# Optimization experiments

Hardware: AMD Instinct MI355X
Metric: run time of the kernel (lower is better)

## Reference

```python
import jax, jax.numpy as jnp
import numpy as np

W = 1024          # hpm.W (Fourier window size)
D = 2 * W         # real-ified dimension
BATCH = 2048
P = 8             # number of previous windows
OMEGA = 50        # sparsity level kept by hard threshold
N_ITERS = 10
L = 1.0           # hpm.L (Lipschitz constant, non-learnable)
CLAMP = 150.0


def setup_inputs() -> dict:
    key = jax.random.key(0)
    k1, k2, k3 = jax.random.split(key, 3)
    x = jax.random.normal(k1, (BATCH, D), jnp.float32)
    prev_windows = jax.random.normal(k2, (P, BATCH, D), jnp.float32)
    # learnable dictionary (Fourier-initialized in the original; random orthogonal-ish here)
    W_d = jax.random.normal(k3, (D, D), jnp.float32) / np.float32(np.sqrt(D))
    # S = I - (1/L) W_d^T W_d, exactly as in __init__
    S = jnp.eye(D, dtype=jnp.float32) - (1.0 / L) * (W_d.T @ W_d)
    lambda2 = jnp.array(1.0, jnp.float32)
    return {"x": x, "prev_windows": prev_windows, "W_d": W_d, "S": S, "lambda2": lambda2}


def _hard_thr(v):
    # keep the OMEGA largest-|.| entries along the last axis, zero the rest
    a = jnp.abs(v)
    kth = jax.lax.top_k(a, OMEGA)[0][..., -1:]  # (batch, 1) threshold
    return jnp.where(a >= kth, v, jnp.zeros_like(v))


def reference(x, prev_windows, W_d, S, lambda2):
    # B = (1/L) W_d x         (batch, D); z vectors kept as (batch, D), last dim == the
    # original dim=-2 since trailing singleton dim is squeezed away.
    B = (1.0 / L) * jnp.einsum('ij,bj->bi', W_d, x)
    z = _hard_thr(B)
    z = _hard_thr(B + jnp.einsum('ij,bj->bi', S, z))

    # attention over previous windows
    s_t = jnp.einsum('ji,bj->bi', W_d, z)                       # W_d^T z : (batch, D)
    s_prev = jnp.einsum('ij,pbj->pbi', W_d, prev_windows)       # (P, batch, D)
    # diagonal of (P,batch,batch) matmul == per-(p,b) dot product; compute it directly
    att = jnp.einsum('pbd,bd->pb', s_prev, s_t)                 # (P, batch)
    att = jax.nn.softmax(att, axis=1)
    pw = jnp.clip(prev_windows, -CLAMP, CLAMP)
    z = lambda2 * jnp.sum(pw * att[..., None], axis=0)          # (batch, D)

    # LIHT iterations; only zs[-1] is used downstream, so carry only the last z
    def step(zc, _):
        zn = _hard_thr(B + jnp.einsum('ij,bj->bi', S, zc))
        return zn, None
    z_last, _ = jax.lax.scan(step, z, None, length=N_ITERS)

    # complex power spectrum: sign flip on imag part does not change the norm
    cpx = z_last.reshape(BATCH, 2, W)
    p = cpx[:, 0, :] ** 2 + cpx[:, 1, :] ** 2                   # (batch, W)
    mD = p.sum(0)                                               # (W,)
    mD_norm = (mD - mD.min()) / (mD.max() - mD.min() + 1e-8)
    return mD_norm, z_last
```

## Files before the change

### kernel.cpp

```cpp
#include <hip/hip_runtime.h>


#define DD 2048
#define NB 2048
#define PLANE ((size_t)1 << 22)
#define ZONE 49152

using short8v  = __attribute__((ext_vector_type(8))) short;
using ushort8v = __attribute__((ext_vector_type(8))) unsigned short;
using ushort4v = __attribute__((ext_vector_type(4))) unsigned short;
using float4v  = __attribute__((ext_vector_type(4))) float;

__device__ __forceinline__ unsigned short f2bf(float f) {
  unsigned u = __float_as_uint(f);
  u = u + 0x7fffu + ((u >> 16) & 1u);
  return (unsigned short)(u >> 16);
}
__device__ __forceinline__ float bf2f(unsigned short h) {
  return __uint_as_float((unsigned)h << 16);
}
__device__ __forceinline__ void gload16(const void* g, void* l) {
  __builtin_amdgcn_global_load_lds((const __attribute__((address_space(1))) void*)g,
                                   (__attribute__((address_space(3))) void*)l,
                                   16, 0, 0);
}

template<int R>
__global__ __launch_bounds__(256)
void conv3T(const float* __restrict__ in, unsigned short* __restrict__ p0,
            unsigned short* __restrict__ p1, unsigned short* __restrict__ p2) {
  __shared__ unsigned short lds3[3][4][R][8];
  const int rt = blockIdx.x, c = blockIdx.y, t = threadIdx.x;
  const int cf = (t & 7) * 4;
  const int g = cf >> 3, e0 = cf & 7;
#pragma unroll
  for (int pass = 0; pass < R / 32; ++pass) {
    const int r = pass * 32 + (t >> 3);
    float4 v = *(const float4*)(in + (size_t)(rt * R + r) * DD + c * 32 + cf);
    float vv[4] = {v.x, v.y, v.z, v.w};
    ushort4v o0, o1, o2;
#pragma unroll
    for (int j = 0; j < 4; ++j) {
      unsigned short a0 = f2bf(vv[j]); float r1 = vv[j] - bf2f(a0);
      unsigned short a1 = f2bf(r1);    float r2 = r1 - bf2f(a1);
      unsigned short a2 = f2bf(r2);
      o0[j] = a0; o1[j] = a1; o2[j] = a2;
    }
    *(ushort4v*)&lds3[0][g][r][e0] = o0;
    *(ushort4v*)&lds3[1][g][r][e0] = o1;
    *(ushort4v*)&lds3[2][g][r][e0] = o2;
  }
  __syncthreads();
  const ushort8v* src = (const ushort8v*)lds3;
  const size_t tb = ((size_t)rt * 64 + c) * (R * 32);
#pragma unroll
  for (int w = 0; w < (3 * R) / 64; ++w) {
    const int idx = w * 256 + t;
    const int p = idx / (4 * R), off = idx % (4 * R);
    unsigned short* dst = (p == 0 ? p0 : p == 1 ? p1 : p2) + tb + (size_t)off * 8;
    *(ushort8v*)dst = src[idx];
  }
}

__global__ __launch_bounds__(256)
void tconv3(const float* __restrict__ in, unsigned short* __restrict__ p0,
            unsigned short* __restrict__ p1, unsigned short* __restrict__ p2) {
  __shared__ unsigned short lds3[3][4][64][8];
  const int nt = blockIdx.x, c = blockIdx.y, t = threadIdx.x;
  const int nf = (t & 15) * 4;
#pragma unroll
  for (int pass = 0; pass < 2; ++pass) {
    const int kr = pass * 16 + (t >> 4);
    float4 v = *(const float4*)(in + (size_t)(c * 32 + kr) * DD + nt * 64 + nf);
    float vv[4] = {v.x, v.y, v.z, v.w};
    const int g = kr >> 3, e = kr & 7;
#pragma unroll
    for (int j = 0; j < 4; ++j) {
      unsigned short a0 = f2bf(vv[j]); float r1 = vv[j] - bf2f(a0);
      unsigned short a1 = f2bf(r1);    float r2 = r1 - bf2f(a1);
      unsigned short a2 = f2bf(r2);
      lds3[0][g][nf + j][e] = a0;
      lds3[1][g][nf + j][e] = a1;
      lds3[2][g][nf + j][e] = a2;
    }
  }
  __syncthreads();
  const ushort8v* src = (const ushort8v*)lds3;
  const size_t tb = ((size_t)nt * 64 + c) * 2048;
#pragma unroll
  for (int w = 0; w < 3; ++w) {
    const int idx = w * 256 + t;
    const int p = idx >> 8, off = idx & 255;
    unsigned short* dst = (p == 0 ? p0 : p == 1 ? p1 : p2) + tb + (size_t)off * 8;
    *(ushort8v*)dst = src[idx];
  }
}

template<int ADD>
__global__ __launch_bounds__(512)
void gemm_bf6(const unsigned short* __restrict__ PA,
              const unsigned short* __restrict__ PB,
              const float* __restrict__ Cadd, float* __restrict__ Cout) {
  __shared__ char lds[3 * ZONE];
  const int tid = threadIdx.x, lane = tid & 63, wid = tid >> 6;

  const int lin = (int)blockIdx.x;
  const int xcd = lin & 7, q = lin >> 3;
  const int mt = (xcd >> 1) * 4 + (q >> 3);
  const int nt = (xcd & 1) * 8 + (q & 7);
  const int m0 = mt * 128, n0 = nt * 128;

  auto stage = [&](char* base, int c) {
    if (wid < 4) {
      const size_t at = ((size_t)mt * 64 + c) * 4096;
#pragma unroll
      for (int i = 0; i < 6; ++i) {
        const int slot = wid * 6 + i, p = slot >> 3, j = slot & 7;
        gload16(PA + p * PLANE + at + j * 512 + lane * 8,
                base + p * 8192 + j * 1024 + lane * 16);
      }
    } else {
#pragma unroll
      for (int i = 0; i < 6; ++i) {
        const int b = (wid - 4) * 6 + i, p = b >> 3, r = b & 7;
        const int sub = r >> 2, j = r & 3;
        const size_t bt = ((size_t)(nt * 2 + sub) * 64 + c) * 2048;
        gload16(PB + p * PLANE + bt + j * 512 + lane * 8,
                base + 24576 + p * 8192 + sub * 4096 + j * 1024 + lane * 16);
      }
    }
  };

  float4v acc[4][2] = {};

  const int rsel = (wid >> 2) * 64;
  const int csel = (wid & 3) * 32;
  const int g16  = lane >> 4;
  const int l15  = lane & 15;
  const int aoff = g16 * 2048 + (rsel + l15) * 16;
  const int boff = 24576 + (csel >> 6) * 4096 + g16 * 1024
                 + ((csel & 32) + l15) * 16;

  stage(lds, 0);
  stage(lds + ZONE, 1);

  int zc = 0, zs = 2;
  for (int c = 0; c < 64; ++c) {
    if (c + 2 < 64) stage(lds + zs * ZONE, c + 2);
    if (c + 2 < 64)      asm volatile("s_waitcnt vmcnt(12)" ::: "memory");
    else if (c + 1 < 64) asm volatile("s_waitcnt vmcnt(6)"  ::: "memory");
    else                 asm volatile("s_waitcnt vmcnt(0)"  ::: "memory");
    __builtin_amdgcn_s_barrier();
    __builtin_amdgcn_sched_barrier(0);

    const char* cur = lds + zc * ZONE;
    short8v b0[2], b1[2], b2[2];
#pragma unroll
    for (int ng = 0; ng < 2; ++ng) {
      b0[ng] = *(const short8v*)(cur + boff + 0 * 8192 + ng * 256);
      b1[ng] = *(const short8v*)(cur + boff + 1 * 8192 + ng * 256);
      b2[ng] = *(const short8v*)(cur + boff + 2 * 8192 + ng * 256);
    }
#pragma unroll
    for (int mg = 0; mg < 4; ++mg) {
      const short8v a0 = *(const short8v*)(cur + 0 * 8192 + aoff + mg * 256);
      const short8v a1 = *(const short8v*)(cur + 1 * 8192 + aoff + mg * 256);
      const short8v a2 = *(const short8v*)(cur + 2 * 8192 + aoff + mg * 256);
#pragma unroll
      for (int ng = 0; ng < 2; ++ng) {
        float4v t = acc[mg][ng];
        t = __builtin_amdgcn_mfma_f32_16x16x32_bf16(a0, b0[ng], t, 0, 0, 0);
        t = __builtin_amdgcn_mfma_f32_16x16x32_bf16(a0, b1[ng], t, 0, 0, 0);
        t = __builtin_amdgcn_mfma_f32_16x16x32_bf16(a1, b0[ng], t, 0, 0, 0);
        t = __builtin_amdgcn_mfma_f32_16x16x32_bf16(a1, b1[ng], t, 0, 0, 0);
        t = __builtin_amdgcn_mfma_f32_16x16x32_bf16(a0, b2[ng], t, 0, 0, 0);
        t = __builtin_amdgcn_mfma_f32_16x16x32_bf16(a2, b0[ng], t, 0, 0, 0);
        acc[mg][ng] = t;
      }
    }
    __builtin_amdgcn_sched_barrier(0);
    __builtin_amdgcn_s_barrier();
    zc = (zc == 2) ? 0 : zc + 1;
    zs = (zs == 2) ? 0 : zs + 1;
  }

  const int row0 = m0 + rsel + g16 * 4;
  const int col0 = n0 + csel + l15;
#pragma unroll
  for (int mg = 0; mg < 4; ++mg)
#pragma unroll
    for (int ng = 0; ng < 2; ++ng)
#pragma unroll
      for (int r = 0; r < 4; ++r) {
        const size_t o = (size_t)(row0 + mg * 16 + r) * DD + col0 + ng * 16;
        float v = acc[mg][ng][r];
        if (ADD) v += Cadd[o];
        Cout[o] = v;
      }
}

template<int HASBASE>
__global__ __launch_bounds__(64)
void spapply_sl(const float* __restrict__ M, const float* __restrict__ baseB,
                float* __restrict__ outF, const unsigned* __restrict__ sidx,
                const float* __restrict__ sval, const int* __restrict__ scnt) {
  const int b = blockIdx.y, lane = threadIdx.x;
  const int col = blockIdx.x * 256 + lane * 4;
  const int nc = scnt[b];
  const unsigned* ip = sidx + b * 64;
  const float* vp = sval + b * 64;
  const size_t ro = (size_t)b * DD + col;
  float4 a;
  if (HASBASE) a = *(const float4*)&baseB[ro];
  else         a = make_float4(0.f, 0.f, 0.f, 0.f);
  for (int t = 0; t < nc; ++t) {
    const unsigned j = ip[t];
    const float v = vp[t];
    float4 m = *(const float4*)&M[(size_t)j * DD + col];
    a.x = fmaf(v, m.x, a.x); a.y = fmaf(v, m.y, a.y);
    a.z = fmaf(v, m.z, a.z); a.w = fmaf(v, m.w, a.w);
  }
  *(float4*)&outF[ro] = a;
}

__global__ __launch_bounds__(64)
void topk_kernel(const float* __restrict__ src, unsigned* __restrict__ sidx,
                 float* __restrict__ sval, int* __restrict__ scnt,
                 float* __restrict__ dense, float* __restrict__ mD,
                 int finalMode) {
  const int b = blockIdx.x;
  const int lane = threadIdx.x;
  const float* row = src + (size_t)b * DD;
  float v[32]; unsigned ab[32];
#pragma unroll
  for (int e4 = 0; e4 < 8; ++e4) {
    float4 t = *(const float4*)&row[e4*256 + lane*4];
    v[e4*4+0]=t.x; v[e4*4+1]=t.y; v[e4*4+2]=t.z; v[e4*4+3]=t.w;
  }
#pragma unroll
  for (int e = 0; e < 32; ++e) ab[e] = __float_as_uint(v[e]) & 0x7fffffffu;

  unsigned mxb = 0;
#pragma unroll
  for (int e = 0; e < 32; ++e) mxb = ab[e] > mxb ? ab[e] : mxb;
  for (int off = 32; off; off >>= 1) {
    unsigned o = (unsigned)__shfl_down((int)mxb, off);
    mxb = o > mxb ? o : mxb;
  }
  mxb = (unsigned)__shfl((int)mxb, 0);
  const int emax = (int)(mxb >> 23);

  int eStar = 0, cntAbove = 0;
  {
    int prevc = 0;
    for (int e = emax; e >= 0; --e) {
      unsigned T = ((unsigned)e) << 23;
      int c = 0;
#pragma unroll
      for (int k = 0; k < 32; ++k) c += (ab[k] >= T) ? 1 : 0;
      for (int off = 32; off; off >>= 1) c += __shfl_down(c, off);
      c = __shfl(c, 0);
      if (c >= 50) { eStar = e; cntAbove = prevc; break; }
      prevc = c;
    }
  }
  unsigned kth = ((unsigned)eStar) << 23;
  int kneed = 50 - cntAbove;

  __shared__ int hist[256];
  __shared__ int sh_sel, sh_kneed;
  for (int p = 0; p < 3; ++p) {
    const unsigned mask = (p==0) ? 0x7F800000u : (p==1) ? 0x7FFF8000u : 0x7FFFFF80u;
    const int sh = (p==0) ? 15 : (p==1) ? 7 : 0;
    for (int t = lane; t < 256; t += 64) hist[t] = 0;
    __syncthreads();
#pragma unroll
    for (int e = 0; e < 32; ++e)
      if ((ab[e] & mask) == kth) atomicAdd(&hist[(ab[e] >> sh) & 0xFF], 1);
    __syncthreads();
    int h0 = hist[lane*4+0], h1 = hist[lane*4+1], h2 = hist[lane*4+2], h3 = hist[lane*4+3];
    int s = h0 + h1 + h2 + h3;
    int x = s;
    for (int off = 1; off < 64; off <<= 1) {
      int y = __shfl_down(x, off);
      if (lane + off < 64) x += y;
    }
    int excl = x - s;
    int c3 = excl + h3, c2 = c3 + h2, c1 = c2 + h1, c0 = c1 + h0;
    if (c0 >= kneed && c1   < kneed) { sh_sel = lane*4+0; sh_kneed = kneed - c1;  }
    if (c1 >= kneed && c2   < kneed) { sh_sel = lane*4+1; sh_kneed = kneed - c2;  }
    if (c2 >= kneed && c3   < kneed) { sh_sel = lane*4+2; sh_kneed = kneed - c3;  }
    if (c3 >= kneed && excl < kneed) { sh_sel = lane*4+3; sh_kneed = kneed - excl;}
    __syncthreads();
    kth |= ((unsigned)sh_sel) << sh;
    kneed = sh_kneed;
    __syncthreads();
  }

  int base = 0;
#pragma unroll
  for (int e4 = 0; e4 < 8; ++e4) {
    float o[4];
#pragma unroll
    for (int qq = 0; qq < 4; ++qq) {
      const int e = e4*4 + qq;
      const bool sel = ab[e] >= kth;
      unsigned long long msk = __ballot(sel);
      int pre = __popcll(msk & ((1ull << lane) - 1ull));
      const unsigned gi = (unsigned)(e4*256 + lane*4 + qq);
      if (sel) {
        int slot = base + pre;
        if (slot < 64) { sidx[b*64+slot] = gi; sval[b*64+slot] = v[e]; }
        if (finalMode) atomicAdd(&mD[gi & 1023u], v[e]*v[e]);
      }
      base += __popcll(msk);
      o[qq] = sel ? v[e] : 0.f;
    }
    if (finalMode) {
      float4 t = {o[0],o[1],o[2],o[3]};
      *(float4*)&dense[(size_t)b*DD + e4*256 + lane*4] = t;
    }
  }
  if (lane == 0) scnt[b] = base < 64 ? base : 64;
}

__global__ __launch_bounds__(256)
void attdot_kernel(const float* __restrict__ prev, const float* __restrict__ U,
                   float* __restrict__ att) {
  const int b = blockIdx.x, p = blockIdx.y, tid = threadIdx.x;
  const float* pr = prev + ((size_t)p*NB + b) * DD;
  const float* u  = U + (size_t)b * DD;
  float s = 0.f;
#pragma unroll
  for (int h = 0; h < 2; ++h) {
    int i = (tid + h*256) * 4;
    float4 a = *(const float4*)&pr[i];
    float4 c = *(const float4*)&u[i];
    s += a.x*c.x + a.y*c.y + a.z*c.z + a.w*c.w;
  }
  for (int off = 32; off; off >>= 1) s += __shfl_down(s, off);
  __shared__ float ps[4];
  if ((tid & 63) == 0) ps[tid >> 6] = s;
  __syncthreads();
  if (tid == 0) att[(size_t)p*NB + b] = ps[0]+ps[1]+ps[2]+ps[3];
}

__global__ __launch_bounds__(256)
void softmax_kernel(const float* __restrict__ att, float* __restrict__ attw) {
  const int p = blockIdx.x, tid = threadIdx.x;
  const float* a = att + (size_t)p*NB;
  float loc[8]; float mx = -3.4e38f;
#pragma unroll
  for (int h = 0; h < 8; ++h) { loc[h] = a[tid + h*256]; mx = fmaxf(mx, loc[h]); }
  for (int off = 32; off; off >>= 1) mx = fmaxf(mx, __shfl_down(mx, off));
  __shared__ float ps[4]; __shared__ float sh_m, sh_s;
  if ((tid & 63) == 0) ps[tid >> 6] = mx;
  __syncthreads();
  if (tid == 0) sh_m = fmaxf(fmaxf(ps[0],ps[1]), fmaxf(ps[2],ps[3]));
  __syncthreads();
  const float m = sh_m;
  float sum = 0.f;
#pragma unroll
  for (int h = 0; h < 8; ++h) sum += expf(loc[h] - m);
  for (int off = 32; off; off >>= 1) sum += __shfl_down(sum, off);
  __syncthreads();
  if ((tid & 63) == 0) ps[tid >> 6] = sum;
  __syncthreads();
  if (tid == 0) sh_s = ps[0]+ps[1]+ps[2]+ps[3];
  __syncthreads();
  const float inv = 1.0f / sh_s;
#pragma unroll
  for (int h = 0; h < 8; ++h) attw[(size_t)p*NB + tid + h*256] = expf(loc[h] - m) * inv;
}

__global__ __launch_bounds__(256)
void zatt_kernel(const float* __restrict__ prev, const float* __restrict__ attw,
                 const float* __restrict__ lam, float* __restrict__ Z) {
  const int b = blockIdx.x, tid = threadIdx.x;
  __shared__ float w[8];
  if (tid < 8) w[tid] = attw[(size_t)tid*NB + b];
  __syncthreads();
  const float l2 = lam[0];
#pragma unroll
  for (int h = 0; h < 2; ++h) {
    int i = (tid + h*256) * 4;
    float4 acc = {0.f,0.f,0.f,0.f};
#pragma unroll
    for (int p = 0; p < 8; ++p) {
      float4 pv = *(const float4*)&prev[((size_t)p*NB + b)*DD + i];
      float wp = w[p];
      acc.x += wp * fminf(fmaxf(pv.x, -150.f), 150.f);
      acc.y += wp * fminf(fmaxf(pv.y, -150.f), 150.f);
      acc.z += wp * fminf(fmaxf(pv.z, -150.f), 150.f);
      acc.w += wp * fminf(fmaxf(pv.w, -150.f), 150.f);
    }
    acc.x *= l2; acc.y *= l2; acc.z *= l2; acc.w *= l2;
    *(float4*)&Z[(size_t)b*DD + i] = acc;
  }
}

__global__ __launch_bounds__(256)
void norm_kernel(float* __restrict__ mD) {
  const int tid = threadIdx.x;
  float v[4]; float mn = 3.4e38f, mx = -3.4e38f;
#pragma unroll
  for (int h = 0; h < 4; ++h) {
    v[h] = mD[tid + h*256];
    mn = fminf(mn, v[h]); mx = fmaxf(mx, v[h]);
  }
  for (int off = 32; off; off >>= 1) {
    mn = fminf(mn, __shfl_down(mn, off));
    mx = fmaxf(mx, __shfl_down(mx, off));
  }
  __shared__ float pmn[4], pmx[4]; __shared__ float smn, smx;
  if ((tid & 63) == 0) { pmn[tid>>6] = mn; pmx[tid>>6] = mx; }
  __syncthreads();
  if (tid == 0) {
    smn = fminf(fminf(pmn[0],pmn[1]), fminf(pmn[2],pmn[3]));
    smx = fmaxf(fmaxf(pmx[0],pmx[1]), fmaxf(pmx[2],pmx[3]));
  }
  __syncthreads();
  const float d = smx - smn + 1e-8f;
#pragma unroll
  for (int h = 0; h < 4; ++h) mD[tid + h*256] = (v[h] - smn) / d;
}

extern "C" void kernel_launch(void* const* d_in, const int* in_sizes, int n_in,
                              void* d_out, int out_size, void* d_ws, size_t ws_size,
                              hipStream_t stream) {
  const float* x    = (const float*)d_in[0];
  const float* prev = (const float*)d_in[1];
  const float* Wd   = (const float*)d_in[2];
  const float* S    = (const float*)d_in[3];
  const float* lam  = (const float*)d_in[4];

  float* out   = (float*)d_out;
  float* mD    = out;
  float* zlast = out + 1024;

  float* B  = (float*)d_ws;
  float* C  = B  + (1u << 22);
  float* X1 = C  + (1u << 22);
  unsigned* sidx = (unsigned*)(X1 + (1u << 22));
  float*    sval = (float*)(sidx + 2048*64);
  int*      scnt = (int*)(sval + 2048*64);
  float*    att  = (float*)(scnt + 2048);
  float*    attw = att + 8*2048;
  unsigned short* PA = (unsigned short*)(attw + 8*2048);
  unsigned short* PB = PA + 3 * PLANE;
  float* U = zlast;

  const dim3 gSp(8, NB);
  const dim3 gA(16, 64);
  const dim3 gB(32, 64);

  conv3T<128><<<gA, 256, 0, stream>>>(x,  PA, PA + PLANE, PA + 2*PLANE);
  conv3T<64> <<<gB, 256, 0, stream>>>(Wd, PB, PB + PLANE, PB + 2*PLANE);
  gemm_bf6<0><<<256, 512, 0, stream>>>(PA, PB, nullptr, B);
  topk_kernel<<<NB, 64, 0, stream>>>(B, sidx, sval, scnt, nullptr, nullptr, 0);
  spapply_sl<1><<<gSp, 64, 0, stream>>>(S, B, C, sidx, sval, scnt);
  topk_kernel<<<NB, 64, 0, stream>>>(C, sidx, sval, scnt, nullptr, nullptr, 0);
  spapply_sl<0><<<gSp, 64, 0, stream>>>(Wd, nullptr, X1, sidx, sval, scnt);
  conv3T<128><<<gA, 256, 0, stream>>>(X1, PA, PA + PLANE, PA + 2*PLANE);
  tconv3<<<gB, 256, 0, stream>>>(Wd, PB, PB + PLANE, PB + 2*PLANE);
  gemm_bf6<0><<<256, 512, 0, stream>>>(PA, PB, nullptr, U);
  attdot_kernel<<<dim3(NB, 8), 256, 0, stream>>>(prev, U, att);
  softmax_kernel<<<8, 256, 0, stream>>>(att, attw);
  zatt_kernel<<<NB, 256, 0, stream>>>(prev, attw, lam, X1);
  conv3T<128><<<gA, 256, 0, stream>>>(X1, PA, PA + PLANE, PA + 2*PLANE);
  conv3T<64> <<<gB, 256, 0, stream>>>(S,  PB, PB + PLANE, PB + 2*PLANE);
  gemm_bf6<1><<<256, 512, 0, stream>>>(PA, PB, B, C);
  topk_kernel<<<NB, 64, 0, stream>>>(C, sidx, sval, scnt, nullptr, nullptr, 0);
  for (int it = 1; it < 10; ++it) {
    spapply_sl<1><<<gSp, 64, 0, stream>>>(S, B, C, sidx, sval, scnt);
    const int fin = (it == 9);
    if (fin) hipMemsetAsync(mD, 0, 1024 * sizeof(float), stream);
    topk_kernel<<<NB, 64, 0, stream>>>(C, sidx, sval, scnt,
                                       fin ? zlast : nullptr,
                                       fin ? mD : nullptr, fin);
  }
  norm_kernel<<<1, 256, 0, stream>>>(mD);
}
```

Measured before the change: 1.218 ms.

## Split GEMM mainloop into half-phase interleaved staging; batch rows in sparse apply

The bf16x3 GEMM mainloop now splits each K-chunk into two halves. Each half loads part of the A fragments, issues half of the next-next stage's global-to-LDS copies, and runs the MFMAs at raised wave priority, so global loads are spread across the compute. Separately, the sparse-apply kernel handles four rows per 256-thread block, stages the index and value lists in LDS, and software-pipelines the gathered row loads four deep to keep more memory requests in flight. The GEMM gains extra barriers per iteration, and the vmcnt accounting must match the new load split.

```diff
diff --git a/kernel.cpp b/kernel.cpp
--- a/kernel.cpp
+++ b/kernel.cpp
@@ -110,19 +110,19 @@
   const int nt = (xcd & 1) * 8 + (q & 7);
   const int m0 = mt * 128, n0 = nt * 128;
 
-  auto stage = [&](char* base, int c) {
+  auto stageH = [&](char* base, int c, int h) {
     if (wid < 4) {
       const size_t at = ((size_t)mt * 64 + c) * 4096;
 #pragma unroll
-      for (int i = 0; i < 6; ++i) {
-        const int slot = wid * 6 + i, p = slot >> 3, j = slot & 7;
+      for (int i = 0; i < 3; ++i) {
+        const int slot = wid * 6 + h * 3 + i, p = slot >> 3, j = slot & 7;
         gload16(PA + p * PLANE + at + j * 512 + lane * 8,
                 base + p * 8192 + j * 1024 + lane * 16);
       }
     } else {
 #pragma unroll
-      for (int i = 0; i < 6; ++i) {
-        const int b = (wid - 4) * 6 + i, p = b >> 3, r = b & 7;
+      for (int i = 0; i < 3; ++i) {
+        const int bb = (wid - 4) * 6 + h * 3 + i, p = bb >> 3, r = bb & 7;
         const int sub = r >> 2, j = r & 3;
         const size_t bt = ((size_t)(nt * 2 + sub) * 64 + c) * 2048;
         gload16(PB + p * PLANE + bt + j * 512 + lane * 8,
@@ -141,19 +141,17 @@
   const int boff = 24576 + (csel >> 6) * 4096 + g16 * 1024
                  + ((csel & 32) + l15) * 16;
 
-  stage(lds, 0);
-  stage(lds + ZONE, 1);
+  stageH(lds, 0, 0);        stageH(lds, 0, 1);
+  stageH(lds + ZONE, 1, 0); stageH(lds + ZONE, 1, 1);
+  asm volatile("s_waitcnt vmcnt(6)" ::: "memory");
+  __builtin_amdgcn_s_barrier();
+  __builtin_amdgcn_sched_barrier(0);
 
   int zc = 0, zs = 2;
   for (int c = 0; c < 64; ++c) {
-    if (c + 2 < 64) stage(lds + zs * ZONE, c + 2);
-    if (c + 2 < 64)      asm volatile("s_waitcnt vmcnt(12)" ::: "memory");
-    else if (c + 1 < 64) asm volatile("s_waitcnt vmcnt(6)"  ::: "memory");
-    else                 asm volatile("s_waitcnt vmcnt(0)"  ::: "memory");
-    __builtin_amdgcn_s_barrier();
-    __builtin_amdgcn_sched_barrier(0);
-
     const char* cur = lds + zc * ZONE;
+    char* nxt = lds + zs * ZONE;
+
     short8v b0[2], b1[2], b2[2];
 #pragma unroll
     for (int ng = 0; ng < 2; ++ng) {
@@ -161,25 +159,66 @@
       b1[ng] = *(const short8v*)(cur + boff + 1 * 8192 + ng * 256);
       b2[ng] = *(const short8v*)(cur + boff + 2 * 8192 + ng * 256);
     }
-#pragma unroll
-    for (int mg = 0; mg < 4; ++mg) {
-      const short8v a0 = *(const short8v*)(cur + 0 * 8192 + aoff + mg * 256);
-      const short8v a1 = *(const short8v*)(cur + 1 * 8192 + aoff + mg * 256);
-      const short8v a2 = *(const short8v*)(cur + 2 * 8192 + aoff + mg * 256);
+    short8v A0[2], A1[2], A2[2];
+#pragma unroll
+    for (int mg = 0; mg < 2; ++mg) {
+      A0[mg] = *(const short8v*)(cur + 0 * 8192 + aoff + mg * 256);
+      A1[mg] = *(const short8v*)(cur + 1 * 8192 + aoff + mg * 256);
+      A2[mg] = *(const short8v*)(cur + 2 * 8192 + aoff + mg * 256);
+    }
+    if (c + 2 < 64) stageH(nxt, c + 2, 0);
+    __builtin_amdgcn_s_barrier();
+    asm volatile("s_waitcnt lgkmcnt(0)" ::: "memory");
+    __builtin_amdgcn_sched_barrier(0);
+    __builtin_amdgcn_s_setprio(1);
+#pragma unroll
+    for (int mg = 0; mg < 2; ++mg)
 #pragma unroll
       for (int ng = 0; ng < 2; ++ng) {
         float4v t = acc[mg][ng];
-        t = __builtin_amdgcn_mfma_f32_16x16x32_bf16(a0, b0[ng], t, 0, 0, 0);
-        t = __builtin_amdgcn_mfma_f32_16x16x32_bf16(a0, b1[ng], t, 0, 0, 0);
-        t = __builtin_amdgcn_mfma_f32_16x16x32_bf16(a1, b0[ng], t, 0, 0, 0);
-        t = __builtin_amdgcn_mfma_f32_16x16x32_bf16(a1, b1[ng], t, 0, 0, 0);
-        t = __builtin_amdgcn_mfma_f32_16x16x32_bf16(a0, b2[ng], t, 0, 0, 0);
-        t = __builtin_amdgcn_mfma_f32_16x16x32_bf16(a2, b0[ng], t, 0, 0, 0);
+        t = __builtin_amdgcn_mfma_f32_16x16x32_bf16(A0[mg], b0[ng], t, 0, 0, 0);
+        t = __builtin_amdgcn_mfma_f32_16x16x32_bf16(A0[mg], b1[ng], t, 0, 0, 0);
+        t = __builtin_amdgcn_mfma_f32_16x16x32_bf16(A1[mg], b0[ng], t, 0, 0, 0);
+        t = __builtin_amdgcn_mfma_f32_16x16x32_bf16(A1[mg], b1[ng], t, 0, 0, 0);
+        t = __builtin_amdgcn_mfma_f32_16x16x32_bf16(A0[mg], b2[ng], t, 0, 0, 0);
+        t = __builtin_amdgcn_mfma_f32_16x16x32_bf16(A2[mg], b0[ng], t, 0, 0, 0);
         acc[mg][ng] = t;
       }
-    }
+    __builtin_amdgcn_s_setprio(0);
     __builtin_amdgcn_sched_barrier(0);
     __builtin_amdgcn_s_barrier();
+
+    short8v C0[2], C1[2], C2[2];
+#pragma unroll
+    for (int mg = 0; mg < 2; ++mg) {
+      C0[mg] = *(const short8v*)(cur + 0 * 8192 + aoff + (mg + 2) * 256);
+      C1[mg] = *(const short8v*)(cur + 1 * 8192 + aoff + (mg + 2) * 256);
+      C2[mg] = *(const short8v*)(cur + 2 * 8192 + aoff + (mg + 2) * 256);
+    }
+    if (c + 2 < 64) stageH(nxt, c + 2, 1);
+    if (c + 2 < 64)      asm volatile("s_waitcnt vmcnt(6)" ::: "memory");
+    else if (c + 1 < 64) asm volatile("s_waitcnt vmcnt(0)" ::: "memory");
+    __builtin_amdgcn_s_barrier();
+    asm volatile("s_waitcnt lgkmcnt(0)" ::: "memory");
+    __builtin_amdgcn_sched_barrier(0);
+    __builtin_amdgcn_s_setprio(1);
+#pragma unroll
+    for (int mg = 0; mg < 2; ++mg)
+#pragma unroll
+      for (int ng = 0; ng < 2; ++ng) {
+        float4v t = acc[mg + 2][ng];
+        t = __builtin_amdgcn_mfma_f32_16x16x32_bf16(C0[mg], b0[ng], t, 0, 0, 0);
+        t = __builtin_amdgcn_mfma_f32_16x16x32_bf16(C0[mg], b1[ng], t, 0, 0, 0);
+        t = __builtin_amdgcn_mfma_f32_16x16x32_bf16(C1[mg], b0[ng], t, 0, 0, 0);
+        t = __builtin_amdgcn_mfma_f32_16x16x32_bf16(C1[mg], b1[ng], t, 0, 0, 0);
+        t = __builtin_amdgcn_mfma_f32_16x16x32_bf16(C0[mg], b2[ng], t, 0, 0, 0);
+        t = __builtin_amdgcn_mfma_f32_16x16x32_bf16(C2[mg], b0[ng], t, 0, 0, 0);
+        acc[mg + 2][ng] = t;
+      }
+    __builtin_amdgcn_s_setprio(0);
+    __builtin_amdgcn_sched_barrier(0);
+    __builtin_amdgcn_s_barrier();
+
     zc = (zc == 2) ? 0 : zc + 1;
     zs = (zs == 2) ? 0 : zs + 1;
   }
@@ -200,25 +239,49 @@
 }
 
 template<int HASBASE>
-__global__ __launch_bounds__(64)
+__global__ __launch_bounds__(256)
 void spapply_sl(const float* __restrict__ M, const float* __restrict__ baseB,
                 float* __restrict__ outF, const unsigned* __restrict__ sidx,
                 const float* __restrict__ sval, const int* __restrict__ scnt) {
-  const int b = blockIdx.y, lane = threadIdx.x;
+  const int lane = threadIdx.x & 63, w = threadIdx.x >> 6;
+  const int b = blockIdx.y * 4 + w;
   const int col = blockIdx.x * 256 + lane * 4;
+  __shared__ unsigned sj[4][64];
+  __shared__ float    sv[4][64];
+  sj[w][lane] = sidx[b * 64 + lane];
+  sv[w][lane] = sval[b * 64 + lane];
   const int nc = scnt[b];
-  const unsigned* ip = sidx + b * 64;
-  const float* vp = sval + b * 64;
+  __syncthreads();
+
   const size_t ro = (size_t)b * DD + col;
   float4 a;
   if (HASBASE) a = *(const float4*)&baseB[ro];
   else         a = make_float4(0.f, 0.f, 0.f, 0.f);
-  for (int t = 0; t < nc; ++t) {
-    const unsigned j = ip[t];
-    const float v = vp[t];
-    float4 m = *(const float4*)&M[(size_t)j * DD + col];
+
+  const float* Mc = M + col;
+  auto ld = [&](int t) -> float4 {
+    return *(const float4*)(Mc + (size_t)sj[w][t] * DD);
+  };
+  auto fma4 = [&](int t, const float4& m) {
+    const float v = sv[w][t];
     a.x = fmaf(v, m.x, a.x); a.y = fmaf(v, m.y, a.y);
     a.z = fmaf(v, m.z, a.z); a.w = fmaf(v, m.w, a.w);
+  };
+
+  int t = 0;
+  if (nc >= 4) {
+    float4 m0 = ld(0), m1 = ld(1), m2 = ld(2), m3 = ld(3);
+    for (; t + 8 <= nc; t += 4) {
+      float4 n0 = ld(t + 4), n1 = ld(t + 5), n2 = ld(t + 6), n3 = ld(t + 7);
+      fma4(t + 0, m0); fma4(t + 1, m1); fma4(t + 2, m2); fma4(t + 3, m3);
+      m0 = n0; m1 = n1; m2 = n2; m3 = n3;
+    }
+    fma4(t + 0, m0); fma4(t + 1, m1); fma4(t + 2, m2); fma4(t + 3, m3);
+    t += 4;
+  }
+  for (; t < nc; ++t) {
+    float4 m = ld(t);
+    fma4(t, m);
   }
   *(float4*)&outF[ro] = a;
 }
@@ -450,7 +513,7 @@
   unsigned short* PB = PA + 3 * PLANE;
   float* U = zlast;
 
-  const dim3 gSp(8, NB);
+  const dim3 gSp(8, NB / 4);
   const dim3 gA(16, 64);
   const dim3 gB(32, 64);
 
@@ -458,9 +521,9 @@
   conv3T<64> <<<gB, 256, 0, stream>>>(Wd, PB, PB + PLANE, PB + 2*PLANE);
   gemm_bf6<0><<<256, 512, 0, stream>>>(PA, PB, nullptr, B);
   topk_kernel<<<NB, 64, 0, stream>>>(B, sidx, sval, scnt, nullptr, nullptr, 0);
-  spapply_sl<1><<<gSp, 64, 0, stream>>>(S, B, C, sidx, sval, scnt);
+  spapply_sl<1><<<gSp, 256, 0, stream>>>(S, B, C, sidx, sval, scnt);
   topk_kernel<<<NB, 64, 0, stream>>>(C, sidx, sval, scnt, nullptr, nullptr, 0);
-  spapply_sl<0><<<gSp, 64, 0, stream>>>(Wd, nullptr, X1, sidx, sval, scnt);
+  spapply_sl<0><<<gSp, 256, 0, stream>>>(Wd, nullptr, X1, sidx, sval, scnt);
   conv3T<128><<<gA, 256, 0, stream>>>(X1, PA, PA + PLANE, PA + 2*PLANE);
   tconv3<<<gB, 256, 0, stream>>>(Wd, PB, PB + PLANE, PB + 2*PLANE);
   gemm_bf6<0><<<256, 512, 0, stream>>>(PA, PB, nullptr, U);
@@ -472,7 +535,7 @@
   gemm_bf6<1><<<256, 512, 0, stream>>>(PA, PB, B, C);
   topk_kernel<<<NB, 64, 0, stream>>>(C, sidx, sval, scnt, nullptr, nullptr, 0);
   for (int it = 1; it < 10; ++it) {
-    spapply_sl<1><<<gSp, 64, 0, stream>>>(S, B, C, sidx, sval, scnt);
+    spapply_sl<1><<<gSp, 256, 0, stream>>>(S, B, C, sidx, sval, scnt);
     const int fin = (it == 9);
     if (fin) hipMemsetAsync(mD, 0, 1024 * sizeof(float), stream);
     topk_kernel<<<NB, 64, 0, stream>>>(C, sidx, sval, scnt,
```

After: 1.096 ms. 1.11x faster.
